# Optimization experiments

Hardware: AMD Instinct MI355X
Metric: run time of the kernel (lower is better)

## Reference

```python
import jax, jax.numpy as jnp
import numpy as np

B, IMG_DIM, H, W = 2, 256, 64, 64
PC_C, PC_D = 16, 16          # voxel_dim = PC_C * PC_D = 256
VOXEL_DIM = PC_C * PC_D
QK_DIM = 256                 # out_channels of img_conv / voxel_conv


def _conv1x1(x, w, b):
    # x: [B, Cin, H, W], w: [Cout, Cin], b: [Cout]  (1x1 conv == per-pixel matmul)
    return jnp.einsum('bchw,oc->bohw', x, w) + b[None, :, None, None]


def setup_inputs() -> dict:
    key = jax.random.key(0)
    ks = jax.random.split(key, 10)
    s = 0.02
    return {
        'img': jax.random.normal(ks[0], (B, IMG_DIM, H, W), jnp.float32),
        'pc': jax.random.normal(ks[1], (B, PC_D, H, W, PC_C), jnp.float32),  # dense() layout [B,D,H,W,C]
        'img_conv_w': jax.random.normal(ks[2], (QK_DIM, IMG_DIM), jnp.float32) * s,
        'img_conv_b': jnp.zeros((QK_DIM,), jnp.float32),
        'voxel_conv_w': jax.random.normal(ks[3], (QK_DIM, VOXEL_DIM), jnp.float32) * s,
        'voxel_conv_b': jnp.zeros((QK_DIM,), jnp.float32),
        'img_v_w': jax.random.normal(ks[4], (IMG_DIM, IMG_DIM), jnp.float32) * s,
        'img_v_b': jnp.zeros((IMG_DIM,), jnp.float32),
        'voxel_v_w': jax.random.normal(ks[5], (VOXEL_DIM, VOXEL_DIM), jnp.float32) * s,
        'voxel_v_b': jnp.zeros((VOXEL_DIM,), jnp.float32),
    }


def reference(img, pc, img_conv_w, img_conv_b, voxel_conv_w, voxel_conv_b,
              img_v_w, img_v_b, voxel_v_w, voxel_v_b):
    b, c_img, h, w = img.shape
    # pc.dense() -> permute(0,4,1,2,3) -> [B, C, D, H, W] -> [B, C*D, H, W]
    pc = jnp.transpose(pc, (0, 4, 1, 2, 3))
    pcb, pcc, pcd, pch, pcw = pc.shape
    pc2 = pc.reshape(pcb, pcc * pcd, pch, pcw)
    n = h * w  # == pch * pcw (required by the bmms)

    img_q = _conv1x1(img, img_conv_w, img_conv_b).reshape(b, QK_DIM, n).transpose(0, 2, 1)  # [B, N, 256]
    pc_k = _conv1x1(pc2, voxel_conv_w, voxel_conv_b).reshape(b, QK_DIM, n)                  # [B, 256, N]
    # unscaled single-head cross attention, softmax over voxel positions
    attn = jax.nn.softmax(jnp.einsum('bnc,bcm->bnm', img_q, pc_k), axis=-1)                 # [B, N_img, N_pc]

    img_v = _conv1x1(img, img_v_w, img_v_b).reshape(b, c_img, n)                            # [B, C_img, N]
    img_v = jnp.einsum('bcn,bmn->bcm', img_v, attn).reshape(b, c_img, h, w)                 # img_v @ attn^T

    pc_v = _conv1x1(pc2, voxel_v_w, voxel_v_b).reshape(b, pcc * pcd, n)                     # [B, C*D, N]
    pc_v = jnp.einsum('bcn,bmn->bcm', pc_v, attn).reshape(b, pcc, pcd, pch, pcw)
    return (img_v, pc_v)
```

## Files before the change

### kernel.cpp

```cpp
#include <hip/hip_runtime.h>
#include <hip/hip_bf16.h>


typedef __hip_bfloat16 bf16;
typedef __attribute__((ext_vector_type(8))) short bf16x8;
typedef __attribute__((ext_vector_type(4))) float f32x4;

#define AS1 __attribute__((address_space(1)))
#define AS3 __attribute__((address_space(3)))

__device__ __forceinline__ void gld_lds16(const bf16* g, bf16* s) {
    __builtin_amdgcn_global_load_lds((const AS1 void*)g, (AS3 void*)s, 16, 0, 0);
}

__device__ __forceinline__ bf16x8 cvt8(const float* __restrict__ p) {
    const float4 a = *(const float4*)p;
    const float4 b = *(const float4*)(p + 4);
    bf16 t[8];
    t[0] = __float2bfloat16(a.x); t[1] = __float2bfloat16(a.y);
    t[2] = __float2bfloat16(a.z); t[3] = __float2bfloat16(a.w);
    t[4] = __float2bfloat16(b.x); t[5] = __float2bfloat16(b.y);
    t[6] = __float2bfloat16(b.z); t[7] = __float2bfloat16(b.w);
    return *(const bf16x8*)t;
}

__global__ __launch_bounds__(256) void proj_kernel(
    const float* __restrict__ img, const float* __restrict__ pc,
    const float* __restrict__ Wq,  const float* __restrict__ bq,
    const float* __restrict__ Wk,  const float* __restrict__ bk,
    const float* __restrict__ Wvi, const float* __restrict__ bvi,
    const float* __restrict__ Wvp, const float* __restrict__ bvp,
    bf16* __restrict__ Qw, bf16* __restrict__ Ktw, bf16* __restrict__ Vall)
{
    __shared__ __align__(16) bf16 XT[64][264];

    const int blk = blockIdx.x;
    const int s   = blk >> 8;
    const int b   = (blk >> 7) & 1;
    const int g   = (blk >> 6) & 1;
    const int n0  = (blk & 63) * 64;
    const int tid = threadIdx.x;

    if (s == 0) {
        const float* src = img + b * 1048576;
        for (int k = 0; k < 16; k++) {
            const int i = tid + k * 256;
            const int cin = i >> 4, nl4 = (i & 15) * 4;
            const float4 v = *(const float4*)&src[cin * 4096 + n0 + nl4];
            XT[nl4 + 0][cin] = __float2bfloat16(v.x);
            XT[nl4 + 1][cin] = __float2bfloat16(v.y);
            XT[nl4 + 2][cin] = __float2bfloat16(v.z);
            XT[nl4 + 3][cin] = __float2bfloat16(v.w);
        }
    } else {
        const float* src = pc + b * 1048576;
        for (int k = 0; k < 16; k++) {
            const int d = k, u = tid;
            const int nl = u >> 2, c4 = (u & 3) * 4;
            const float4 v = *(const float4*)&src[d * 65536 + (n0 + nl) * 16 + c4];
            XT[nl][(c4 + 0) * 16 + d] = __float2bfloat16(v.x);
            XT[nl][(c4 + 1) * 16 + d] = __float2bfloat16(v.y);
            XT[nl][(c4 + 2) * 16 + d] = __float2bfloat16(v.z);
            XT[nl][(c4 + 3) * 16 + d] = __float2bfloat16(v.w);
        }
    }
    __syncthreads();

    const float* W = s ? (g ? Wvp : Wk) : (g ? Wvi : Wq);
    const float* Bv = s ? (g ? bvp : bk) : (g ? bvi : bq);

    const int wv = tid >> 6, lane = tid & 63, l16 = lane & 15, quad = lane >> 4;
    const int ob = wv * 64;

    f32x4 acc[4][4] = {};

    for (int ks = 0; ks < 8; ks++) {
        const int k0 = ks * 32;
        bf16x8 af[4], wf[4];
        for (int ti = 0; ti < 4; ti++)
            af[ti] = *(const bf16x8*)&XT[ti * 16 + l16][k0 + quad * 8];
        for (int tj = 0; tj < 4; tj++)
            wf[tj] = cvt8(&W[(ob + tj * 16 + l16) * 256 + k0 + quad * 8]);
        for (int ti = 0; ti < 4; ti++)
            for (int tj = 0; tj < 4; tj++)
                acc[ti][tj] = __builtin_amdgcn_mfma_f32_16x16x32_bf16(af[ti], wf[tj], acc[ti][tj], 0, 0, 0);
    }

    if (g == 0) {
        bf16* D1 = (s ? Ktw : Qw) + b * (4096 * 256);
        for (int tj = 0; tj < 4; tj++) {
            const int o = ob + tj * 16 + l16;
            const float bias = Bv[o];
            for (int ti = 0; ti < 4; ti++) {
                const int nl = ti * 16 + quad * 4;
                for (int r = 0; r < 4; r++)
                    D1[(n0 + nl + r) * 256 + o] = __float2bfloat16(acc[ti][tj][r] + bias);
            }
        }
    } else {
        bf16* D2 = Vall + b * (512 * 4096) + (s ? 256 * 4096 : 0);
        for (int tj = 0; tj < 4; tj++) {
            const int o = ob + tj * 16 + l16;
            const float bias = Bv[o];
            for (int ti = 0; ti < 4; ti++) {
                const int nl = ti * 16 + quad * 4;
                bf16 pv[4];
                for (int r = 0; r < 4; r++)
                    pv[r] = __float2bfloat16(acc[ti][tj][r] + bias);
                *(uint2*)&D2[o * 4096 + n0 + nl] = *(const uint2*)pv;
            }
        }
    }
}

__global__ __launch_bounds__(256) void attn_s_kernel(
    const bf16* __restrict__ Qw, const bf16* __restrict__ Ktw,
    bf16* __restrict__ Pt, float* __restrict__ Lpart)
{
    __shared__ __align__(16) bf16 As[128 * 32];
    __shared__ __align__(16) bf16 Bs[128 * 32];

    const int b  = blockIdx.z;
    const int q0 = blockIdx.y * 128;
    const int p0 = blockIdx.x * 128;
    const bf16* A = Qw  + b * (4096 * 256);
    const bf16* B = Ktw + b * (4096 * 256);

    const int tid = threadIdx.x;
    const int wv = tid >> 6, lane = tid & 63, l16 = lane & 15, quad = lane >> 4;
    const int wr = wv >> 1, wc = wv & 1;

    f32x4 acc[4][4] = {};

    for (int ks = 0; ks < 8; ks++) {
        const int k0 = ks * 32;
        bf16x8 av[2], bv[2];
        for (int c = 0; c < 2; c++) {
            const int ci = c * 256 + tid;
            const int row = ci >> 2, kc = ci & 3;
            av[c] = *(const bf16x8*)&A[(q0 + row) * 256 + k0 + kc * 8];
            bv[c] = *(const bf16x8*)&B[(p0 + row) * 256 + k0 + kc * 8];
        }
        __syncthreads();
        for (int c = 0; c < 2; c++) {
            const int ci = c * 256 + tid;
            *(bf16x8*)&As[ci * 8] = av[c];
            *(bf16x8*)&Bs[ci * 8] = bv[c];
        }
        __syncthreads();
        bf16x8 af[4], bfr[4];
        for (int t = 0; t < 4; t++) {
            af[t]  = *(const bf16x8*)&As[(wr * 64 + t * 16 + l16) * 32 + quad * 8];
            bfr[t] = *(const bf16x8*)&Bs[(wc * 64 + t * 16 + l16) * 32 + quad * 8];
        }
        for (int ti = 0; ti < 4; ti++)
            for (int tj = 0; tj < 4; tj++)
                acc[ti][tj] = __builtin_amdgcn_mfma_f32_16x16x32_bf16(af[ti], bfr[tj], acc[ti][tj], 0, 0, 0);
    }

    bf16* Pdst = Pt + (size_t)b * 4096 * 4096;
    const int strip = blockIdx.x * 2 + wc;
    for (int ti = 0; ti < 4; ti++) {
        for (int r = 0; r < 4; r++) {
            const int qrow = wr * 64 + ti * 16 + quad * 4 + r;
            const int q = q0 + qrow;
            float partial = 0.0f;
            for (int tj = 0; tj < 4; tj++) {
                const float e = __expf(fminf(acc[ti][tj][r], 80.0f));
                partial += e;
                Pdst[(size_t)q * 4096 + p0 + wc * 64 + tj * 16 + l16] = __float2bfloat16(e);
            }
            partial += __shfl_xor(partial, 1);
            partial += __shfl_xor(partial, 2);
            partial += __shfl_xor(partial, 4);
            partial += __shfl_xor(partial, 8);
            if (l16 == 0)
                Lpart[(size_t)(b * 4096 + q) * 64 + strip] = partial;
        }
    }
}

__global__ __launch_bounds__(256) void lred_kernel(
    const float* __restrict__ Lpart, float* __restrict__ Linv)
{
    const int row = blockIdx.x * 256 + threadIdx.x;
    const float4* lp = (const float4*)&Lpart[(size_t)row * 64];
    float s = 0.0f;
    for (int i = 0; i < 16; i++) {
        const float4 v = lp[i];
        s += v.x + v.y + v.z + v.w;
    }
    Linv[row] = 1.0f / fmaxf(s, 1e-30f);
}

__global__ __launch_bounds__(256) void attn_o_kernel(
    const bf16* __restrict__ Vall, const bf16* __restrict__ Pt,
    const float* __restrict__ Linv, float* __restrict__ out)
{
    __shared__ __align__(16) bf16 As[128 * 32];
    __shared__ __align__(16) bf16 Bs[64 * 32];

    const int b  = blockIdx.z;
    const int c0 = blockIdx.y * 128;
    const int q0 = blockIdx.x * 64;
    const bf16* A = Vall + (size_t)b * 512 * 4096;
    const bf16* B = Pt   + (size_t)b * 4096 * 4096;

    const int tid = threadIdx.x;
    const int wv = tid >> 6, lane = tid & 63, l16 = lane & 15, quad = lane >> 4;
    const int wr = wv >> 1, wc = wv & 1;

    f32x4 acc[4][2] = {};

    const int arow = tid >> 2, akc = tid & 3;
    for (int ks = 0; ks < 128; ks++) {
        const int k0 = ks * 32;
        gld_lds16(A + (c0 + arow) * 4096 + k0 + akc * 8, As + tid * 8);
        gld_lds16(A + (c0 + 64 + arow) * 4096 + k0 + akc * 8, As + 2048 + tid * 8);
        gld_lds16(B + (q0 + arow) * 4096 + k0 + akc * 8, Bs + tid * 8);
        __syncthreads();
        bf16x8 af[4], bfr[2];
        for (int t = 0; t < 4; t++)
            af[t]  = *(const bf16x8*)&As[(wr * 64 + t * 16 + l16) * 32 + quad * 8];
        for (int t = 0; t < 2; t++)
            bfr[t] = *(const bf16x8*)&Bs[(wc * 32 + t * 16 + l16) * 32 + quad * 8];
        for (int ti = 0; ti < 4; ti++)
            for (int tj = 0; tj < 2; tj++)
                acc[ti][tj] = __builtin_amdgcn_mfma_f32_16x16x32_bf16(af[ti], bfr[tj], acc[ti][tj], 0, 0, 0);
        __syncthreads();
    }

    float rl[2];
    for (int tj = 0; tj < 2; tj++)
        rl[tj] = Linv[b * 4096 + q0 + wc * 32 + tj * 16 + l16];

    for (int ti = 0; ti < 4; ti++) {
        for (int r = 0; r < 4; r++) {
            const int c_ = c0 + wr * 64 + ti * 16 + quad * 4 + r;
            const size_t base = (c_ < 256)
                ? ((size_t)b * 1048576 + (size_t)c_ * 4096)
                : (2097152u + (size_t)b * 1048576 + (size_t)(c_ - 256) * 4096);
            for (int tj = 0; tj < 2; tj++) {
                const int q = q0 + wc * 32 + tj * 16 + l16;
                out[base + q] = acc[ti][tj][r] * rl[tj];
            }
        }
    }
}

extern "C" void kernel_launch(void* const* d_in, const int* in_sizes, int n_in,
                              void* d_out, int out_size, void* d_ws, size_t ws_size,
                              hipStream_t stream)
{
    const float* img = (const float*)d_in[0];
    const float* pc  = (const float*)d_in[1];
    const float* Wq  = (const float*)d_in[2];
    const float* bq  = (const float*)d_in[3];
    const float* Wk  = (const float*)d_in[4];
    const float* bk  = (const float*)d_in[5];
    const float* Wvi = (const float*)d_in[6];
    const float* bvi = (const float*)d_in[7];
    const float* Wvp = (const float*)d_in[8];
    const float* bvp = (const float*)d_in[9];

    char* ws = (char*)d_ws;
    bf16*  Qw    = (bf16*)(ws);
    bf16*  Ktw   = (bf16*)(ws + (4ull  << 20));
    bf16*  Vall  = (bf16*)(ws + (8ull  << 20));
    bf16*  Pt    = (bf16*)(ws + (16ull << 20));
    float* Lpart = (float*)(ws + (80ull << 20));
    float* Linv  = (float*)(ws + (82ull << 20));

    proj_kernel<<<512, 256, 0, stream>>>(img, pc, Wq, bq, Wk, bk,
                                         Wvi, bvi, Wvp, bvp, Qw, Ktw, Vall);
    attn_s_kernel<<<dim3(32, 32, 2), 256, 0, stream>>>(Qw, Ktw, Pt, Lpart);
    lred_kernel<<<32, 256, 0, stream>>>(Lpart, Linv);
    attn_o_kernel<<<dim3(64, 4, 2), 256, 0, stream>>>(Vall, Pt, Linv, (float*)d_out);
}
```

Measured before the change: 212.0 us.

## Split-K attention output GEMM with direct-to-LDS loads and transposed P layout

Several coordinated changes. The Q/K projection now swaps MFMA operands so it can write vectorized 4-element stores. The score kernel now stages tiles through global_load_lds with a swizzled chunk layout and writes P transposed with packed stores. The output GEMM becomes a split-K kernel over 128x128 tiles, writing fp32 partials, followed by a reduce kernel that sums them and applies the softmax normalization. This targets low occupancy and poor load efficiency in the output GEMM, at the cost of extra fp32 partial traffic and an extra launch. The old path is kept as a fallback when the workspace is too small.

```diff
diff --git a/kernel.cpp b/kernel.cpp
--- a/kernel.cpp
+++ b/kernel.cpp
@@ -22,6 +22,10 @@
     t[4] = __float2bfloat16(b.x); t[5] = __float2bfloat16(b.y);
     t[6] = __float2bfloat16(b.z); t[7] = __float2bfloat16(b.w);
     return *(const bf16x8*)t;
+}
+
+__device__ __forceinline__ int chunk_of(int row, int kc) {
+    return ((row >> 3) << 5) + (kc << 3) + (row & 7);
 }
 
 __global__ __launch_bounds__(256) void proj_kernel(
@@ -66,7 +70,7 @@
     }
     __syncthreads();
 
-    const float* W = s ? (g ? Wvp : Wk) : (g ? Wvi : Wq);
+    const float* W  = s ? (g ? Wvp : Wk) : (g ? Wvi : Wq);
     const float* Bv = s ? (g ? bvp : bk) : (g ? bvi : bq);
 
     const int wv = tid >> 6, lane = tid & 63, l16 = lane & 15, quad = lane >> 4;
@@ -81,20 +85,30 @@
             af[ti] = *(const bf16x8*)&XT[ti * 16 + l16][k0 + quad * 8];
         for (int tj = 0; tj < 4; tj++)
             wf[tj] = cvt8(&W[(ob + tj * 16 + l16) * 256 + k0 + quad * 8]);
-        for (int ti = 0; ti < 4; ti++)
-            for (int tj = 0; tj < 4; tj++)
-                acc[ti][tj] = __builtin_amdgcn_mfma_f32_16x16x32_bf16(af[ti], wf[tj], acc[ti][tj], 0, 0, 0);
+        if (g == 0) {
+            for (int ti = 0; ti < 4; ti++)
+                for (int tj = 0; tj < 4; tj++)
+                    acc[ti][tj] = __builtin_amdgcn_mfma_f32_16x16x32_bf16(wf[tj], af[ti], acc[ti][tj], 0, 0, 0);
+        } else {
+            for (int ti = 0; ti < 4; ti++)
+                for (int tj = 0; tj < 4; tj++)
+                    acc[ti][tj] = __builtin_amdgcn_mfma_f32_16x16x32_bf16(af[ti], wf[tj], acc[ti][tj], 0, 0, 0);
+        }
     }
 
     if (g == 0) {
         bf16* D1 = (s ? Ktw : Qw) + b * (4096 * 256);
         for (int tj = 0; tj < 4; tj++) {
-            const int o = ob + tj * 16 + l16;
-            const float bias = Bv[o];
+            const int o0 = ob + tj * 16 + quad * 4;
+            const float4 bi = *(const float4*)&Bv[o0];
             for (int ti = 0; ti < 4; ti++) {
-                const int nl = ti * 16 + quad * 4;
-                for (int r = 0; r < 4; r++)
-                    D1[(n0 + nl + r) * 256 + o] = __float2bfloat16(acc[ti][tj][r] + bias);
+                const int n = n0 + ti * 16 + l16;
+                bf16 pv[4];
+                pv[0] = __float2bfloat16(acc[ti][tj][0] + bi.x);
+                pv[1] = __float2bfloat16(acc[ti][tj][1] + bi.y);
+                pv[2] = __float2bfloat16(acc[ti][tj][2] + bi.z);
+                pv[3] = __float2bfloat16(acc[ti][tj][3] + bi.w);
+                *(uint2*)&D1[n * 256 + o0] = *(const uint2*)pv;
             }
         }
     } else {
@@ -121,61 +135,64 @@
     __shared__ __align__(16) bf16 Bs[128 * 32];
 
     const int b  = blockIdx.z;
+    const int p0 = blockIdx.x * 128;
     const int q0 = blockIdx.y * 128;
-    const int p0 = blockIdx.x * 128;
-    const bf16* A = Qw  + b * (4096 * 256);
-    const bf16* B = Ktw + b * (4096 * 256);
+    const bf16* A = Ktw + b * (4096 * 256);
+    const bf16* B = Qw  + b * (4096 * 256);
 
     const int tid = threadIdx.x;
     const int wv = tid >> 6, lane = tid & 63, l16 = lane & 15, quad = lane >> 4;
     const int wr = wv >> 1, wc = wv & 1;
 
+    const int srow = ((tid >> 5) << 3) | (tid & 7);
+    const int skc  = (tid >> 3) & 3;
+
     f32x4 acc[4][4] = {};
 
     for (int ks = 0; ks < 8; ks++) {
         const int k0 = ks * 32;
-        bf16x8 av[2], bv[2];
-        for (int c = 0; c < 2; c++) {
-            const int ci = c * 256 + tid;
-            const int row = ci >> 2, kc = ci & 3;
-            av[c] = *(const bf16x8*)&A[(q0 + row) * 256 + k0 + kc * 8];
-            bv[c] = *(const bf16x8*)&B[(p0 + row) * 256 + k0 + kc * 8];
-        }
-        __syncthreads();
-        for (int c = 0; c < 2; c++) {
-            const int ci = c * 256 + tid;
-            *(bf16x8*)&As[ci * 8] = av[c];
-            *(bf16x8*)&Bs[ci * 8] = bv[c];
-        }
+        gld_lds16(A + (p0 + srow     ) * 256 + k0 + skc * 8, As + tid * 8);
+        gld_lds16(A + (p0 + 64 + srow) * 256 + k0 + skc * 8, As + (256 + tid) * 8);
+        gld_lds16(B + (q0 + srow     ) * 256 + k0 + skc * 8, Bs + tid * 8);
+        gld_lds16(B + (q0 + 64 + srow) * 256 + k0 + skc * 8, Bs + (256 + tid) * 8);
         __syncthreads();
         bf16x8 af[4], bfr[4];
         for (int t = 0; t < 4; t++) {
-            af[t]  = *(const bf16x8*)&As[(wr * 64 + t * 16 + l16) * 32 + quad * 8];
-            bfr[t] = *(const bf16x8*)&Bs[(wc * 64 + t * 16 + l16) * 32 + quad * 8];
+            const int Ra = wr * 64 + t * 16 + l16;
+            const int Rb = wc * 64 + t * 16 + l16;
+            af[t]  = *(const bf16x8*)&As[chunk_of(Ra, quad) * 8];
+            bfr[t] = *(const bf16x8*)&Bs[chunk_of(Rb, quad) * 8];
         }
         for (int ti = 0; ti < 4; ti++)
             for (int tj = 0; tj < 4; tj++)
                 acc[ti][tj] = __builtin_amdgcn_mfma_f32_16x16x32_bf16(af[ti], bfr[tj], acc[ti][tj], 0, 0, 0);
+        __syncthreads();
     }
 
     bf16* Pdst = Pt + (size_t)b * 4096 * 4096;
-    const int strip = blockIdx.x * 2 + wc;
+    float lsum[4] = {0.f, 0.f, 0.f, 0.f};
     for (int ti = 0; ti < 4; ti++) {
-        for (int r = 0; r < 4; r++) {
-            const int qrow = wr * 64 + ti * 16 + quad * 4 + r;
-            const int q = q0 + qrow;
-            float partial = 0.0f;
-            for (int tj = 0; tj < 4; tj++) {
+        const int pr = p0 + wr * 64 + ti * 16 + quad * 4;
+        for (int tj = 0; tj < 4; tj++) {
+            const int q = q0 + wc * 64 + tj * 16 + l16;
+            bf16 pv[4];
+            float su = 0.0f;
+            for (int r = 0; r < 4; r++) {
                 const float e = __expf(fminf(acc[ti][tj][r], 80.0f));
-                partial += e;
-                Pdst[(size_t)q * 4096 + p0 + wc * 64 + tj * 16 + l16] = __float2bfloat16(e);
+                su += e;
+                pv[r] = __float2bfloat16(e);
             }
-            partial += __shfl_xor(partial, 1);
-            partial += __shfl_xor(partial, 2);
-            partial += __shfl_xor(partial, 4);
-            partial += __shfl_xor(partial, 8);
-            if (l16 == 0)
-                Lpart[(size_t)(b * 4096 + q) * 64 + strip] = partial;
+            lsum[tj] += su;
+            *(uint2*)&Pdst[(size_t)q * 4096 + pr] = *(const uint2*)pv;
+        }
+    }
+    for (int tj = 0; tj < 4; tj++) {
+        float v = lsum[tj];
+        v += __shfl_xor(v, 16);
+        v += __shfl_xor(v, 32);
+        if (quad == 0) {
+            const int q = q0 + wc * 64 + tj * 16 + l16;
+            Lpart[(size_t)(b * 4096 + q) * 64 + blockIdx.x * 2 + wr] = v;
         }
     }
 }
@@ -193,7 +210,84 @@
     Linv[row] = 1.0f / fmaxf(s, 1e-30f);
 }
 
-__global__ __launch_bounds__(256) void attn_o_kernel(
+__global__ __launch_bounds__(256) void attn_o_splitk(
+    const bf16* __restrict__ Pt, const bf16* __restrict__ Vall,
+    float* __restrict__ Opart)
+{
+    __shared__ __align__(16) bf16 As[128 * 32];
+    __shared__ __align__(16) bf16 Bs[128 * 32];
+
+    const int z = blockIdx.z;
+    const int b = z >> 1, s = z & 1;
+    const int q0 = blockIdx.x * 128;
+    const int c0 = blockIdx.y * 128;
+    const bf16* A  = Pt   + (size_t)b * 4096 * 4096;
+    const bf16* Bp = Vall + (size_t)b * 512 * 4096;
+
+    const int tid = threadIdx.x;
+    const int wv = tid >> 6, lane = tid & 63, l16 = lane & 15, quad = lane >> 4;
+    const int wr = wv >> 1, wc = wv & 1;
+
+    const int srow = ((tid >> 5) << 3) | (tid & 7);
+    const int skc  = (tid >> 3) & 3;
+    const int kbase = s * 2048;
+
+    f32x4 acc[4][4] = {};
+
+    for (int ks = 0; ks < 64; ks++) {
+        const int k0 = kbase + ks * 32;
+        gld_lds16(A  + (size_t)(q0 + srow     ) * 4096 + k0 + skc * 8, As + tid * 8);
+        gld_lds16(A  + (size_t)(q0 + 64 + srow) * 4096 + k0 + skc * 8, As + (256 + tid) * 8);
+        gld_lds16(Bp + (size_t)(c0 + srow     ) * 4096 + k0 + skc * 8, Bs + tid * 8);
+        gld_lds16(Bp + (size_t)(c0 + 64 + srow) * 4096 + k0 + skc * 8, Bs + (256 + tid) * 8);
+        __syncthreads();
+        bf16x8 af[4], bfr[4];
+        for (int t = 0; t < 4; t++) {
+            const int Ra = wr * 64 + t * 16 + l16;
+            const int Rb = wc * 64 + t * 16 + l16;
+            af[t]  = *(const bf16x8*)&As[chunk_of(Ra, quad) * 8];
+            bfr[t] = *(const bf16x8*)&Bs[chunk_of(Rb, quad) * 8];
+        }
+        for (int ti = 0; ti < 4; ti++)
+            for (int tj = 0; tj < 4; tj++)
+                acc[ti][tj] = __builtin_amdgcn_mfma_f32_16x16x32_bf16(af[ti], bfr[tj], acc[ti][tj], 0, 0, 0);
+        __syncthreads();
+    }
+
+    float* Od = Opart + (size_t)(s * 2 + b) * 512 * 4096;
+    for (int ti = 0; ti < 4; ti++) {
+        const int q = q0 + wr * 64 + ti * 16 + quad * 4;
+        for (int tj = 0; tj < 4; tj++) {
+            const int c = c0 + wc * 64 + tj * 16 + l16;
+            *(f32x4*)&Od[(size_t)c * 4096 + q] = acc[ti][tj];
+        }
+    }
+}
+
+__global__ __launch_bounds__(256) void reduce_kernel(
+    const float* __restrict__ Opart, const float* __restrict__ Linv,
+    float* __restrict__ out)
+{
+    const int f = blockIdx.x * 256 + threadIdx.x;
+    const size_t g = (size_t)f * 4;
+    const int q4 = (int)(g & 4095);
+    const int c  = (int)((g >> 12) & 511);
+    const int b  = (int)(g >> 21);
+    const float4 a0 = *(const float4*)&Opart[g];
+    const float4 a1 = *(const float4*)&Opart[g + 4194304];
+    const float4 li = *(const float4*)&Linv[b * 4096 + q4];
+    float4 o;
+    o.x = (a0.x + a1.x) * li.x;
+    o.y = (a0.y + a1.y) * li.y;
+    o.z = (a0.z + a1.z) * li.z;
+    o.w = (a0.w + a1.w) * li.w;
+    const size_t base = (c < 256)
+        ? ((size_t)b * 1048576 + (size_t)c * 4096 + q4)
+        : (2097152u + (size_t)b * 1048576 + (size_t)(c - 256) * 4096 + q4);
+    *(float4*)&out[base] = o;
+}
+
+__global__ __launch_bounds__(256) void attn_o_small(
     const bf16* __restrict__ Vall, const bf16* __restrict__ Pt,
     const float* __restrict__ Linv, float* __restrict__ out)
 {
@@ -270,10 +364,16 @@
     bf16*  Pt    = (bf16*)(ws + (16ull << 20));
     float* Lpart = (float*)(ws + (80ull << 20));
     float* Linv  = (float*)(ws + (82ull << 20));
+    float* Opart = (float*)(ws + (83ull << 20));
 
     proj_kernel<<<512, 256, 0, stream>>>(img, pc, Wq, bq, Wk, bk,
                                          Wvi, bvi, Wvp, bvp, Qw, Ktw, Vall);
     attn_s_kernel<<<dim3(32, 32, 2), 256, 0, stream>>>(Qw, Ktw, Pt, Lpart);
     lred_kernel<<<32, 256, 0, stream>>>(Lpart, Linv);
-    attn_o_kernel<<<dim3(64, 4, 2), 256, 0, stream>>>(Vall, Pt, Linv, (float*)d_out);
-}
+    if (ws_size >= (148ull << 20)) {
+        attn_o_splitk<<<dim3(32, 4, 4), 256, 0, stream>>>(Pt, Vall, Opart);
+        reduce_kernel<<<4096, 256, 0, stream>>>(Opart, Linv, (float*)d_out);
+    } else {
+        attn_o_small<<<dim3(64, 4, 2), 256, 0, stream>>>(Vall, Pt, Linv, (float*)d_out);
+    }
+}
```

Result: slower. 231.2 us (+9.0%).
